# Kernel optimization log

Measured on AMD Instinct MI355X. Metric: run time of the kernel, lower is better.

## Reference

```python
import jax, jax.numpy as jnp
import numpy as np

N = 4096        # blocklength == number of checks (code requires square H)
DENSITY = 0.005 # ~20 ones per row/col, typical LDPC sparsity


def setup_inputs() -> dict:
    key = jax.random.key(0)
    k1, k2 = jax.random.split(key)
    # sparse binary parity-check matrix, stored dense as the module does
    H = (jax.random.uniform(k1, (N, N)) < DENSITY).astype(jnp.float32)
    llr = jax.random.normal(k2, (N,), dtype=jnp.float32)
    gamma = jnp.ones((), dtype=jnp.float32)  # learned damping scalar
    return {"llr": llr, "H": H, "gamma": gamma, "n_iter": 5}


def reference(llr, H, gamma, n_iter):
    mask = H != 0                      # jnp.where(H, ...) truthiness
    BIG = jnp.float32(1e9)
    M = H.shape[0]
    v2c = jnp.tile(llr, (M, 1))        # (M, N)
    c2v = None
    for _ in range(n_iter):
        # check-node update: sign via masked matmul, magnitude via masked row-min
        c2v_sign = jnp.sign(H @ jnp.sign(v2c.T))                    # (M, M)
        c2v_mag = jnp.min(jnp.where(mask, jnp.abs(v2c), BIG),       # (M, 1)
                          axis=1, keepdims=True)
        c2v = gamma * c2v_sign * c2v_mag                            # (M, M)
        # variable-node update
        v2c = llr + H.T @ c2v                                       # (N, M)
    return llr + H.T @ c2v                                          # (N, M)
```

## Files before the change

kernel.cpp:

```cpp
#include <hip/hip_runtime.h>


#define KMAX 64
#define SV   56

typedef unsigned int u32;

__device__ __forceinline__ int sgn_i(int x)    { return (x > 0) - (x < 0); }
__device__ __forceinline__ int sgn_f(float x)  { return (x > 0.f) - (x < 0.f); }

__device__ __forceinline__ void acc_bytes(int w, int* a) {
    a[0] += (w << 24) >> 24;
    a[1] += (w << 16) >> 24;
    a[2] += (w << 8) >> 24;
    a[3] += (w >> 24);
}

__device__ __forceinline__ unsigned pack4(int s0, int s1, int s2, int s3) {
    return  (unsigned)(unsigned char)(signed char)s0
         | ((unsigned)(unsigned char)(signed char)s1 << 8)
         | ((unsigned)(unsigned char)(signed char)s2 << 16)
         | ((unsigned)(unsigned char)(signed char)s3 << 24);
}

__device__ __forceinline__ void gload_lds16(const signed char* g, int* l) {
    __builtin_amdgcn_global_load_lds(
        (const __attribute__((address_space(1))) u32*)g,
        (__attribute__((address_space(3))) u32*)l, 16, 0, 0);
}


__global__ void k_transpose_f32(const float* __restrict__ in, float* __restrict__ out, int n) {
    __shared__ float tile[32][33];
    int bx = blockIdx.x * 32, by = blockIdx.y * 32;
    int tx = threadIdx.x, ty = threadIdx.y;
    for (int r = ty; r < 32; r += 8) tile[r][tx] = in[(size_t)(by + r) * n + bx + tx];
    __syncthreads();
    for (int r = ty; r < 32; r += 8) out[(size_t)(bx + r) * n + by + tx] = tile[tx][r];
}

__global__ void k_extract_rows(const float* __restrict__ M, int n,
                               int* __restrict__ cols, int* __restrict__ len) {
    int wave = (int)((blockIdx.x * blockDim.x + threadIdx.x) >> 6);
    int lane = threadIdx.x & 63;
    if (wave >= n) return;
    const float* row = M + (size_t)wave * n;
    int count = 0;
    for (int c0 = 0; c0 < n; c0 += 64) {
        float v = row[c0 + lane];
        unsigned long long ball = __ballot(v != 0.0f);
        int pre = __popcll(ball & ((1ull << lane) - 1ull));
        if (v != 0.0f) {
            int pos = count + pre;
            if (pos < KMAX) cols[wave * KMAX + pos] = c0 + lane;
        }
        count += __popcll(ball);
    }
    if (lane == 0) len[wave] = (count > KMAX) ? KMAX : count;
}

__global__ void k_build_lst(const int* __restrict__ col_rows, const int* __restrict__ col_len,
                            int* __restrict__ lst, int n) {
    int a = (int)((blockIdx.x * blockDim.x + threadIdx.x) >> 6);
    int lane = threadIdx.x & 63;
    if (a >= n) return;
    int len = col_len[a];
    int leaf = 999;
    if (lane < len) leaf = col_rows[a * KMAX + lane] >> 7;
    for (int L = 0; L < 33; ++L) {
        unsigned long long b = __ballot(lane < len && leaf < L);
        if (lane == 0) lst[a * 33 + L] = __popcll(b);
    }
}

__global__ void k_build_tab(const int* __restrict__ col_rows, const int* __restrict__ col_len,
                            const float* __restrict__ magv, int2* __restrict__ tab, int n) {
    int a = (int)((blockIdx.x * blockDim.x + threadIdx.x) >> 6);
    int lane = threadIdx.x & 63;
    if (a >= n) return;
    int len = col_len[a];
    if (lane < KMAX) {
        int2 e = make_int2(0, 0);
        if (lane < len) {
            int mm = col_rows[a * KMAX + lane];
            e = make_int2(mm * n | (mm & 7), __float_as_int(magv[mm]));
        }
        tab[a * KMAX + lane] = e;
    }
}


__global__ void k_init_sgt0(const float* __restrict__ llr, signed char* __restrict__ sgt, int n) {
    int b = blockIdx.x;
    int s = sgn_f(llr[b]);
    unsigned w = (unsigned)(unsigned char)(signed char)s * 0x01010101u;
    int4 val = make_int4((int)w, (int)w, (int)w, (int)w);
    int4* row = (int4*)(sgt + (size_t)b * n);
    for (int t = threadIdx.x; t < n / 16; t += blockDim.x) row[t] = val;
}

__global__ void k_init_wnz0(const float* __restrict__ llr, const int* __restrict__ row_cols,
                            const int* __restrict__ row_len, float* __restrict__ wnz, int n) {
    int m = (int)((blockIdx.x * blockDim.x + threadIdx.x) >> 6);
    int lane = threadIdx.x & 63;
    if (m >= n) return;
    if (lane < row_len[m]) wnz[m * KMAX + lane] = llr[row_cols[m * KMAX + lane]];
}


__global__ void k_check(const signed char* __restrict__ sgt, const float* __restrict__ wnz,
                        const int* __restrict__ row_cols, const int* __restrict__ row_len,
                        const float* __restrict__ gamma, float* __restrict__ magv,
                        signed char* __restrict__ sg1, int n) {
    const int m = blockIdx.x;
    const int tid = threadIdx.x;
    __shared__ int s_cols[KMAX];
    __shared__ int s_len_sh;
    if (tid == 0) s_len_sh = row_len[m];
    __syncthreads();
    const int len = s_len_sh;
    if (tid < KMAX) s_cols[tid] = (tid < len) ? row_cols[m * KMAX + tid] : 0;
    __syncthreads();

    if (tid < 64) {
        float v = (tid < len) ? fabsf(wnz[m * KMAX + tid]) : 1e9f;
        #pragma unroll
        for (int off = 32; off > 0; off >>= 1) v = fminf(v, __shfl_down(v, off));
        if (tid == 0) magv[m] = gamma[0] * v;
    }

    for (int i0 = tid * 16; i0 < n; i0 += blockDim.x * 16) {
        int acc[16];
        #pragma unroll
        for (int k = 0; k < 16; k++) acc[k] = 0;
        for (int t = 0; t < len; t++) {
            const int j = s_cols[t];
            int4 v = *reinterpret_cast<const int4*>(sgt + (size_t)j * n + i0);
            acc_bytes(v.x, acc + 0);
            acc_bytes(v.y, acc + 4);
            acc_bytes(v.z, acc + 8);
            acc_bytes(v.w, acc + 12);
        }
        unsigned o0 = pack4(sgn_i(acc[0]),  sgn_i(acc[1]),  sgn_i(acc[2]),  sgn_i(acc[3]));
        unsigned o1 = pack4(sgn_i(acc[4]),  sgn_i(acc[5]),  sgn_i(acc[6]),  sgn_i(acc[7]));
        unsigned o2 = pack4(sgn_i(acc[8]),  sgn_i(acc[9]),  sgn_i(acc[10]), sgn_i(acc[11]));
        unsigned o3 = pack4(sgn_i(acc[12]), sgn_i(acc[13]), sgn_i(acc[14]), sgn_i(acc[15]));
        *reinterpret_cast<int4*>(sg1 + (size_t)m * n + i0) = make_int4((int)o0, (int)o1, (int)o2, (int)o3);
    }
}

__device__ __forceinline__ float extb(int v, int c) {
    return (float)((v << (24 - 8 * c)) >> 24);
}

__device__ __forceinline__ void leaf4(float lv[4], int t0, int t1, int tid,
                                      const int* __restrict__ s_v,
                                      const int2* __restrict__ ttab) {
    const int cnt = t1 - t0;
    if (cnt == 0) {
        #pragma unroll
        for (int c = 0; c < 4; ++c) lv[c] = 0.f;
        return;
    }
    const int v0 = s_v[t0 * 256 + tid];
    const float w0 = __int_as_float(ttab[t0].y);
    if (cnt == 1) {
        #pragma unroll
        for (int c = 0; c < 4; ++c) lv[c] = w0 * extb(v0, c);
        return;
    }
    const int v1 = s_v[(t0 + 1) * 256 + tid];
    const float w1 = __int_as_float(ttab[t0 + 1].y);
    if (cnt == 2) {
        #pragma unroll
        for (int c = 0; c < 4; ++c) lv[c] = w0 * extb(v0, c) + w1 * extb(v1, c);
        return;
    }
    float r[8][4];
    #pragma unroll
    for (int l = 0; l < 8; ++l) {
        #pragma unroll
        for (int c = 0; c < 4; ++c) r[l][c] = 0.f;
    }
    #define ACCL(l) { _Pragma("unroll") for (int c = 0; c < 4; ++c) r[l][c] += w * extb(v, c); }
    for (int t = t0; t < t1; ++t) {
        int2 e = ttab[t];
        const int v = s_v[t * 256 + tid];
        const float w = __int_as_float(e.y);
        switch (e.x & 7) {
            case 0: ACCL(0); break;
            case 1: ACCL(1); break;
            case 2: ACCL(2); break;
            case 3: ACCL(3); break;
            case 4: ACCL(4); break;
            case 5: ACCL(5); break;
            case 6: ACCL(6); break;
            default: ACCL(7); break;
        }
    }
    #undef ACCL
    #pragma unroll
    for (int c = 0; c < 4; ++c)
        lv[c] = ((r[0][c] + r[1][c]) + (r[2][c] + r[3][c]))
              + ((r[4][c] + r[5][c]) + (r[6][c] + r[7][c]));
}

template <bool LAST>
__global__ __launch_bounds__(256, 2) void k_var(
                      const signed char* __restrict__ sg1,
                      const int2* __restrict__ tab, const int* __restrict__ lst,
                      const float* __restrict__ llr,
                      const int* __restrict__ row_cols, const int* __restrict__ row_len,
                      signed char* __restrict__ sgn, float* __restrict__ wnz,
                      float* __restrict__ wout, int n) {
    extern __shared__ int smem[];
    int* s_v = smem;
    float* s_row = (float*)(smem + SV * 256);
    const int a = blockIdx.x;
    const int q = blockIdx.y;
    const int tid = threadIdx.x;
    const int wid = tid >> 6;
    const int lane = tid & 63;
    const int col4 = q * (n >> 4) + tid;
    const int2* __restrict__ ttab = tab + a * KMAX;
    const int* __restrict__ tlst = lst + a * 33;

    const signed char* qbase = sg1 + q * (n >> 2) + (size_t)lane * 16;
    #pragma unroll
    for (int j = 0; j < SV / 4; ++j) {
        const int t = wid * (SV / 4) + j;
        const int rowoff = ttab[t].x & ~7;
        gload_lds16(qbase + rowoff, s_v + t * 256);
    }
    asm volatile("s_waitcnt vmcnt(0)" ::: "memory");
    __syncthreads();

    int stv[33];
    #pragma unroll
    for (int L = 0; L < 33; ++L) { int s = tlst[L]; stv[L] = (s > SV) ? SV : s; }

    float stk0[4], stk1[4], stk2[4], stk3[4], stk4[4];
    float tot[4];
    #pragma unroll
    for (int L = 0; L < 32; ++L) {
        float cur[4];
        leaf4(cur, stv[L], stv[L + 1], tid, s_v, ttab);
        if (L & 1) {
            #pragma unroll
            for (int c = 0; c < 4; ++c) cur[c] = stk0[c] + cur[c];
        }
        if ((L & 3) == 3) {
            #pragma unroll
            for (int c = 0; c < 4; ++c) cur[c] = stk1[c] + cur[c];
        }
        if ((L & 7) == 7) {
            #pragma unroll
            for (int c = 0; c < 4; ++c) cur[c] = stk2[c] + cur[c];
        }
        if ((L & 15) == 15) {
            #pragma unroll
            for (int c = 0; c < 4; ++c) cur[c] = stk3[c] + cur[c];
        }
        if ((L & 31) == 31) {
            #pragma unroll
            for (int c = 0; c < 4; ++c) cur[c] = stk4[c] + cur[c];
        }
        if (L == 31) {
            #pragma unroll
            for (int c = 0; c < 4; ++c) tot[c] = cur[c];
        } else if ((L & 1) == 0) {
            #pragma unroll
            for (int c = 0; c < 4; ++c) stk0[c] = cur[c];
        } else if ((L & 3) == 1) {
            #pragma unroll
            for (int c = 0; c < 4; ++c) stk1[c] = cur[c];
        } else if ((L & 7) == 3) {
            #pragma unroll
            for (int c = 0; c < 4; ++c) stk2[c] = cur[c];
        } else if ((L & 15) == 7) {
            #pragma unroll
            for (int c = 0; c < 4; ++c) stk3[c] = cur[c];
        } else {
            #pragma unroll
            for (int c = 0; c < 4; ++c) stk4[c] = cur[c];
        }
    }

    float wb[4];
    const float4 l4 = *reinterpret_cast<const float4*>(llr + col4 * 4);
    const float lf[4] = { l4.x, l4.y, l4.z, l4.w };
    #pragma unroll
    for (int c = 0; c < 4; ++c) wb[c] = lf[c] + tot[c];

    if (LAST) {
        *reinterpret_cast<float4*>(wout + (size_t)a * n + col4 * 4) =
            make_float4(wb[0], wb[1], wb[2], wb[3]);
    } else {
        unsigned o = pack4(sgn_f(wb[0]), sgn_f(wb[1]), sgn_f(wb[2]), sgn_f(wb[3]));
        *reinterpret_cast<int*>(sgn + (size_t)a * n + col4 * 4) = (int)o;
        *reinterpret_cast<float4*>(s_row + tid * 4) =
            make_float4(wb[0], wb[1], wb[2], wb[3]);

        __syncthreads();
        if (tid < KMAX) {
            int rl = row_len[a];
            if (tid < rl) {
                int j = row_cols[a * KMAX + tid];
                int qlo = q * (n >> 2);
                if (j >= qlo && j < qlo + (n >> 2))
                    wnz[a * KMAX + tid] = s_row[j - qlo];
            }
        }
    }
}

__global__ void k_transpose_i8_inplace(signed char* __restrict__ A, int n) {
    const int bx = blockIdx.x, by = blockIdx.y;
    if (bx > by) return;
    __shared__ signed char t1[64][68];
    __shared__ signed char t2[64][68];
    const int tid = threadIdx.x;
    const int r = tid >> 2;
    const int c0 = (tid & 3) * 16;
    const size_t o1 = (size_t)(by * 64 + r) * n + bx * 64 + c0;
    const size_t o2 = (size_t)(bx * 64 + r) * n + by * 64 + c0;
    {
        int4 v = *reinterpret_cast<const int4*>(A + o1);
        int* lp = (int*)&t1[r][c0];
        lp[0] = v.x; lp[1] = v.y; lp[2] = v.z; lp[3] = v.w;
    }
    if (bx != by) {
        int4 v = *reinterpret_cast<const int4*>(A + o2);
        int* lp = (int*)&t2[r][c0];
        lp[0] = v.x; lp[1] = v.y; lp[2] = v.z; lp[3] = v.w;
    }
    __syncthreads();
    {
        unsigned o[4];
        #pragma unroll
        for (int q = 0; q < 4; q++) {
            unsigned x0 = (unsigned char)t1[c0 + q * 4 + 0][r];
            unsigned x1 = (unsigned char)t1[c0 + q * 4 + 1][r];
            unsigned x2 = (unsigned char)t1[c0 + q * 4 + 2][r];
            unsigned x3 = (unsigned char)t1[c0 + q * 4 + 3][r];
            o[q] = x0 | (x1 << 8) | (x2 << 16) | (x3 << 24);
        }
        *reinterpret_cast<int4*>(A + o2) = make_int4((int)o[0], (int)o[1], (int)o[2], (int)o[3]);
    }
    if (bx != by) {
        unsigned o[4];
        #pragma unroll
        for (int q = 0; q < 4; q++) {
            unsigned x0 = (unsigned char)t2[c0 + q * 4 + 0][r];
            unsigned x1 = (unsigned char)t2[c0 + q * 4 + 1][r];
            unsigned x2 = (unsigned char)t2[c0 + q * 4 + 2][r];
            unsigned x3 = (unsigned char)t2[c0 + q * 4 + 3][r];
            o[q] = x0 | (x1 << 8) | (x2 << 16) | (x3 << 24);
        }
        *reinterpret_cast<int4*>(A + o1) = make_int4((int)o[0], (int)o[1], (int)o[2], (int)o[3]);
    }
}


extern "C" void kernel_launch(void* const* d_in, const int* in_sizes, int n_in,
                              void* d_out, int out_size, void* d_ws, size_t ws_size,
                              hipStream_t stream) {
    const float* llr   = (const float*)d_in[0];
    const float* H     = (const float*)d_in[1];
    const float* gamma = (const float*)d_in[2];
    const int n = in_sizes[0];
    const int N_ITER = 5;
    (void)ws_size; (void)n_in; (void)out_size;

    char* ws = (char*)d_ws;
    const size_t NB = (size_t)n * (size_t)n;

    signed char* SGA = (signed char*)ws;
    signed char* SGB = (signed char*)(ws + NB);
    char* p = ws + 2 * NB;
    int*   row_cols = (int*)p;   p += (size_t)n * KMAX * 4;
    int*   col_rows = (int*)p;   p += (size_t)n * KMAX * 4;
    float* wnz      = (float*)p; p += (size_t)n * KMAX * 4;
    int2*  tab      = (int2*)p;  p += (size_t)n * KMAX * 8;
    int*   lst      = (int*)p;   p += (size_t)n * 33 * 4;
    int*   row_len  = (int*)p;   p += (size_t)n * 4;
    int*   col_len  = (int*)p;   p += (size_t)n * 4;
    float* magv     = (float*)p; p += (size_t)n * 4;

    float* HT = (float*)d_out;

    {
        dim3 bT(32, 8), gT(n / 32, n / 32);
        k_transpose_f32<<<gT, bT, 0, stream>>>(H, HT, n);
    }
    k_extract_rows<<<n / 4, 256, 0, stream>>>(H, n, row_cols, row_len);
    k_extract_rows<<<n / 4, 256, 0, stream>>>(HT, n, col_rows, col_len);
    k_build_lst<<<n / 4, 256, 0, stream>>>(col_rows, col_len, lst, n);

    k_init_sgt0<<<n, 256, 0, stream>>>(llr, SGA, n);
    k_init_wnz0<<<n / 4, 256, 0, stream>>>(llr, row_cols, row_len, wnz, n);

    const size_t sv_bytes = (size_t)SV * 256 * 4;

    for (int it = 0; it < N_ITER; ++it) {
        k_check<<<n, 256, 0, stream>>>(SGA, wnz, row_cols, row_len, gamma, magv, SGB, n);
        k_build_tab<<<n / 4, 256, 0, stream>>>(col_rows, col_len, magv, tab, n);
        if (it + 1 < N_ITER) {
            k_var<false><<<dim3(n, 4), 256, sv_bytes + (n / 4) * sizeof(float), stream>>>(
                SGB, tab, lst, llr, row_cols, row_len, SGA, wnz, nullptr, n);
            k_transpose_i8_inplace<<<dim3(n / 64, n / 64), 256, 0, stream>>>(SGA, n);
        } else {
            k_var<true><<<dim3(n, 4), 256, sv_bytes, stream>>>(
                SGB, tab, lst, llr, row_cols, row_len, nullptr, nullptr,
                (float*)d_out, n);
        }
    }
}
```

Measured before the change: 1.190 ms.

## Split k_var leaf reduction across 8 threads per column group with shuffle reduce

```diff
diff --git a/kernel.cpp b/kernel.cpp
--- a/kernel.cpp
+++ b/kernel.cpp
@@ -3,6 +3,7 @@
 
 #define KMAX 64
 #define SV   56
+#define SVP  65
 
 typedef unsigned int u32;
 
@@ -23,10 +24,10 @@
          | ((unsigned)(unsigned char)(signed char)s3 << 24);
 }
 
-__device__ __forceinline__ void gload_lds16(const signed char* g, int* l) {
+__device__ __forceinline__ void gload_lds4(const signed char* g, int* l) {
     __builtin_amdgcn_global_load_lds(
         (const __attribute__((address_space(1))) u32*)g,
-        (__attribute__((address_space(3))) u32*)l, 16, 0, 0);
+        (__attribute__((address_space(3))) u32*)l, 4, 0, 0);
 }
 
 
@@ -153,24 +154,25 @@
     return (float)((v << (24 - 8 * c)) >> 24);
 }
 
-__device__ __forceinline__ void leaf4(float lv[4], int t0, int t1, int tid,
+__device__ __forceinline__ void leaf4(float lv[4], int t0, int t1, int d,
                                       const int* __restrict__ s_v,
-                                      const int2* __restrict__ ttab) {
+                                      const float* __restrict__ s_w,
+                                      const int* __restrict__ s_ln) {
     const int cnt = t1 - t0;
     if (cnt == 0) {
         #pragma unroll
         for (int c = 0; c < 4; ++c) lv[c] = 0.f;
         return;
     }
-    const int v0 = s_v[t0 * 256 + tid];
-    const float w0 = __int_as_float(ttab[t0].y);
+    const int v0 = s_v[t0 * SVP + d];
+    const float w0 = s_w[t0];
     if (cnt == 1) {
         #pragma unroll
         for (int c = 0; c < 4; ++c) lv[c] = w0 * extb(v0, c);
         return;
     }
-    const int v1 = s_v[(t0 + 1) * 256 + tid];
-    const float w1 = __int_as_float(ttab[t0 + 1].y);
+    const int v1 = s_v[(t0 + 1) * SVP + d];
+    const float w1 = s_w[t0 + 1];
     if (cnt == 2) {
         #pragma unroll
         for (int c = 0; c < 4; ++c) lv[c] = w0 * extb(v0, c) + w1 * extb(v1, c);
@@ -184,10 +186,9 @@
     }
     #define ACCL(l) { _Pragma("unroll") for (int c = 0; c < 4; ++c) r[l][c] += w * extb(v, c); }
     for (int t = t0; t < t1; ++t) {
-        int2 e = ttab[t];
-        const int v = s_v[t * 256 + tid];
-        const float w = __int_as_float(e.y);
-        switch (e.x & 7) {
+        const int v = s_v[t * SVP + d];
+        const float w = s_w[t];
+        switch (s_ln[t]) {
             case 0: ACCL(0); break;
             case 1: ACCL(1); break;
             case 2: ACCL(2); break;
@@ -206,7 +207,7 @@
 }
 
 template <bool LAST>
-__global__ __launch_bounds__(256, 2) void k_var(
+__global__ __launch_bounds__(512, 4) void k_var(
                       const signed char* __restrict__ sg1,
                       const int2* __restrict__ tab, const int* __restrict__ lst,
                       const float* __restrict__ llr,
@@ -214,101 +215,93 @@
                       signed char* __restrict__ sgn, float* __restrict__ wnz,
                       float* __restrict__ wout, int n) {
     extern __shared__ int smem[];
-    int* s_v = smem;
-    float* s_row = (float*)(smem + SV * 256);
+    int*   s_v  = smem;
+    float* s_w  = (float*)(smem + SV * SVP);
+    int*   s_ln = (int*)(s_w + KMAX);
+    float* s_row = (float*)(s_ln + KMAX);
     const int a = blockIdx.x;
     const int q = blockIdx.y;
     const int tid = threadIdx.x;
     const int wid = tid >> 6;
     const int lane = tid & 63;
-    const int col4 = q * (n >> 4) + tid;
+    const int d = tid >> 3;
+    const int j = tid & 7;
+    const int col4 = q * 64 + d;
     const int2* __restrict__ ttab = tab + a * KMAX;
     const int* __restrict__ tlst = lst + a * 33;
 
-    const signed char* qbase = sg1 + q * (n >> 2) + (size_t)lane * 16;
-    #pragma unroll
-    for (int j = 0; j < SV / 4; ++j) {
-        const int t = wid * (SV / 4) + j;
+    if (tid < KMAX) {
+        int2 e = ttab[tid];
+        s_w[tid] = __int_as_float(e.y);
+        s_ln[tid] = e.x & 7;
+    }
+
+    const signed char* qseg = sg1 + q * 256 + (size_t)lane * 4;
+    #pragma unroll
+    for (int jj = 0; jj < SV / 8; ++jj) {
+        const int t = wid * (SV / 8) + jj;
         const int rowoff = ttab[t].x & ~7;
-        gload_lds16(qbase + rowoff, s_v + t * 256);
+        gload_lds4(qseg + rowoff, s_v + t * SVP);
     }
     asm volatile("s_waitcnt vmcnt(0)" ::: "memory");
     __syncthreads();
 
-    int stv[33];
-    #pragma unroll
-    for (int L = 0; L < 33; ++L) { int s = tlst[L]; stv[L] = (s > SV) ? SV : s; }
-
-    float stk0[4], stk1[4], stk2[4], stk3[4], stk4[4];
-    float tot[4];
-    #pragma unroll
-    for (int L = 0; L < 32; ++L) {
-        float cur[4];
-        leaf4(cur, stv[L], stv[L + 1], tid, s_v, ttab);
-        if (L & 1) {
-            #pragma unroll
-            for (int c = 0; c < 4; ++c) cur[c] = stk0[c] + cur[c];
-        }
-        if ((L & 3) == 3) {
-            #pragma unroll
-            for (int c = 0; c < 4; ++c) cur[c] = stk1[c] + cur[c];
-        }
-        if ((L & 7) == 7) {
-            #pragma unroll
-            for (int c = 0; c < 4; ++c) cur[c] = stk2[c] + cur[c];
-        }
-        if ((L & 15) == 15) {
-            #pragma unroll
-            for (int c = 0; c < 4; ++c) cur[c] = stk3[c] + cur[c];
-        }
-        if ((L & 31) == 31) {
-            #pragma unroll
-            for (int c = 0; c < 4; ++c) cur[c] = stk4[c] + cur[c];
-        }
-        if (L == 31) {
-            #pragma unroll
-            for (int c = 0; c < 4; ++c) tot[c] = cur[c];
-        } else if ((L & 1) == 0) {
-            #pragma unroll
-            for (int c = 0; c < 4; ++c) stk0[c] = cur[c];
-        } else if ((L & 3) == 1) {
-            #pragma unroll
-            for (int c = 0; c < 4; ++c) stk1[c] = cur[c];
-        } else if ((L & 7) == 3) {
-            #pragma unroll
-            for (int c = 0; c < 4; ++c) stk2[c] = cur[c];
-        } else if ((L & 15) == 7) {
-            #pragma unroll
-            for (int c = 0; c < 4; ++c) stk3[c] = cur[c];
+    int b[5];
+    #pragma unroll
+    for (int k = 0; k < 5; ++k) {
+        int s = tlst[4 * j + k];
+        b[k] = (s > SV) ? SV : s;
+    }
+
+    float lvA[4], lvB[4], p01[4], p23[4], qv[4];
+    leaf4(lvA, b[0], b[1], d, s_v, s_w, s_ln);
+    leaf4(lvB, b[1], b[2], d, s_v, s_w, s_ln);
+    #pragma unroll
+    for (int c = 0; c < 4; ++c) p01[c] = lvA[c] + lvB[c];
+    leaf4(lvA, b[2], b[3], d, s_v, s_w, s_ln);
+    leaf4(lvB, b[3], b[4], d, s_v, s_w, s_ln);
+    #pragma unroll
+    for (int c = 0; c < 4; ++c) p23[c] = lvA[c] + lvB[c];
+    #pragma unroll
+    for (int c = 0; c < 4; ++c) qv[c] = p01[c] + p23[c];
+
+    #pragma unroll
+    for (int c = 0; c < 4; ++c) {
+        float o = __shfl_xor(qv[c], 1);
+        qv[c] = (j & 1) ? (o + qv[c]) : (qv[c] + o);
+        o = __shfl_xor(qv[c], 2);
+        qv[c] = (j & 2) ? (o + qv[c]) : (qv[c] + o);
+        o = __shfl_xor(qv[c], 4);
+        qv[c] = (j & 4) ? (o + qv[c]) : (qv[c] + o);
+    }
+
+    if (j == 0) {
+        float wb[4];
+        const float4 l4 = *reinterpret_cast<const float4*>(llr + col4 * 4);
+        const float lf[4] = { l4.x, l4.y, l4.z, l4.w };
+        #pragma unroll
+        for (int c = 0; c < 4; ++c) wb[c] = lf[c] + qv[c];
+
+        if (LAST) {
+            *reinterpret_cast<float4*>(wout + (size_t)a * n + col4 * 4) =
+                make_float4(wb[0], wb[1], wb[2], wb[3]);
         } else {
-            #pragma unroll
-            for (int c = 0; c < 4; ++c) stk4[c] = cur[c];
-        }
-    }
-
-    float wb[4];
-    const float4 l4 = *reinterpret_cast<const float4*>(llr + col4 * 4);
-    const float lf[4] = { l4.x, l4.y, l4.z, l4.w };
-    #pragma unroll
-    for (int c = 0; c < 4; ++c) wb[c] = lf[c] + tot[c];
-
-    if (LAST) {
-        *reinterpret_cast<float4*>(wout + (size_t)a * n + col4 * 4) =
-            make_float4(wb[0], wb[1], wb[2], wb[3]);
-    } else {
-        unsigned o = pack4(sgn_f(wb[0]), sgn_f(wb[1]), sgn_f(wb[2]), sgn_f(wb[3]));
-        *reinterpret_cast<int*>(sgn + (size_t)a * n + col4 * 4) = (int)o;
-        *reinterpret_cast<float4*>(s_row + tid * 4) =
-            make_float4(wb[0], wb[1], wb[2], wb[3]);
-
+            unsigned o = pack4(sgn_f(wb[0]), sgn_f(wb[1]), sgn_f(wb[2]), sgn_f(wb[3]));
+            *reinterpret_cast<int*>(sgn + (size_t)a * n + col4 * 4) = (int)o;
+            *reinterpret_cast<float4*>(s_row + d * 4) =
+                make_float4(wb[0], wb[1], wb[2], wb[3]);
+        }
+    }
+
+    if (!LAST) {
         __syncthreads();
         if (tid < KMAX) {
             int rl = row_len[a];
             if (tid < rl) {
-                int j = row_cols[a * KMAX + tid];
-                int qlo = q * (n >> 2);
-                if (j >= qlo && j < qlo + (n >> 2))
-                    wnz[a * KMAX + tid] = s_row[j - qlo];
+                int jcol = row_cols[a * KMAX + tid];
+                int qlo = q * 256;
+                if (jcol >= qlo && jcol < qlo + 256)
+                    wnz[a * KMAX + tid] = s_row[jcol - qlo];
             }
         }
     }
@@ -400,17 +393,17 @@
     k_init_sgt0<<<n, 256, 0, stream>>>(llr, SGA, n);
     k_init_wnz0<<<n / 4, 256, 0, stream>>>(llr, row_cols, row_len, wnz, n);
 
-    const size_t sv_bytes = (size_t)SV * 256 * 4;
+    const size_t sv_bytes = (size_t)(SV * SVP + KMAX + KMAX + 256) * 4;
 
     for (int it = 0; it < N_ITER; ++it) {
         k_check<<<n, 256, 0, stream>>>(SGA, wnz, row_cols, row_len, gamma, magv, SGB, n);
         k_build_tab<<<n / 4, 256, 0, stream>>>(col_rows, col_len, magv, tab, n);
         if (it + 1 < N_ITER) {
-            k_var<false><<<dim3(n, 4), 256, sv_bytes + (n / 4) * sizeof(float), stream>>>(
+            k_var<false><<<dim3(n, 16), 512, sv_bytes, stream>>>(
                 SGB, tab, lst, llr, row_cols, row_len, SGA, wnz, nullptr, n);
             k_transpose_i8_inplace<<<dim3(n / 64, n / 64), 256, 0, stream>>>(SGA, n);
         } else {
-            k_var<true><<<dim3(n, 4), 256, sv_bytes, stream>>>(
+            k_var<true><<<dim3(n, 16), 512, sv_bytes, stream>>>(
                 SGB, tab, lst, llr, row_cols, row_len, nullptr, nullptr,
                 (float*)d_out, n);
         }
```

After: 2.809 ms. 136% more time.
